# Performance work log

Hardware: AMD Instinct MI355X
Metric: run time of the kernel (lower is better)

The kernel has to match this reference:

```python
import jax, jax.numpy as jnp
import numpy as np

NB, H = 4, 16
EPS = 1e-5


def _ln(x, w=None, b=None):
    m = jnp.mean(x, -1, keepdims=True)
    v = jnp.var(x, -1, keepdims=True)
    y = (x - m) * jax.lax.rsqrt(v + EPS)
    if w is not None:
        y = y * w
    if b is not None:
        y = y + b
    return y


def _ada_ln(a, s, ln_s_w, w_gamma, w_beta):
    # AF3 Algorithm 26: a <- sigmoid(Lin(LN_nobias(s))) * LN_noaffine(a) + Lin(LN_nobias(s))
    a_n = _ln(a)
    s_n = _ln(s, ln_s_w)
    return jax.nn.sigmoid(s_n @ w_gamma) * a_n + s_n @ w_beta


def setup_inputs():
    key = jax.random.key(0)
    B, S, c_a, c_s, c_z = 1, 1024, 768, 384, 128
    n_hidden = 2 * c_a  # expansion factor n=2
    ks = iter(jax.random.split(key, 40))

    def rn(shape, scale=1.0):
        return scale * jax.random.normal(next(ks), shape, dtype=jnp.float32)

    p = 0.02
    return {
        "a": rn((B, S, c_a)),
        "s": rn((B, S, c_s)),
        "z": rn((B, S, S, c_z)),
        "beta": rn((B, S, S, H)),
        # per-block AttentionPairBias params (stacked over NB blocks)
        "ln_s_w_attn": jnp.ones((NB, c_s)),
        "wg_attn": rn((NB, c_s, c_a), p),
        "wb_attn": rn((NB, c_s, c_a), p),
        "wq": rn((NB, c_a, c_a), p),
        "bq": jnp.zeros((NB, c_a)),
        "wk": rn((NB, c_a, c_a), p),
        "wv": rn((NB, c_a, c_a), p),
        "ln_z_w": jnp.ones((NB, c_z)),
        "ln_z_b": jnp.zeros((NB, c_z)),
        "wpb": rn((NB, c_z, H), p),
        "wgate": rn((NB, c_a, c_a), p),
        "wo": rn((NB, c_a, c_a), p),
        "wsg_attn": rn((NB, c_s, c_a), p),
        "bsg_attn": -2.0 * jnp.ones((NB, c_a)),
        # per-block ConditionedTransitionBlock params
        "ln_s_w_tr": jnp.ones((NB, c_s)),
        "wg_tr": rn((NB, c_s, c_a), p),
        "wb_tr": rn((NB, c_s, c_a), p),
        "w_swish": rn((NB, c_a, n_hidden), p),
        "w_gate2": rn((NB, c_a, n_hidden), p),
        "wsg_tr": rn((NB, c_s, c_a), p),
        "bsg_tr": -2.0 * jnp.ones((NB, c_a)),
        "w_out": rn((NB, n_hidden, c_a), p),
    }


def reference(a, s, z, beta, ln_s_w_attn, wg_attn, wb_attn, wq, bq, wk, wv,
              ln_z_w, ln_z_b, wpb, wgate, wo, wsg_attn, bsg_attn,
              ln_s_w_tr, wg_tr, wb_tr, w_swish, w_gate2, wsg_tr, bsg_tr, w_out):
    B, S, c_a = a.shape
    d = c_a // H
    scale = 1.0 / jnp.sqrt(jnp.float32(d))
    for i in range(NB):
        # --- AttentionPairBias (AF3 Alg 24) ---
        ah = _ada_ln(a, s, ln_s_w_attn[i], wg_attn[i], wb_attn[i])
        q = (ah @ wq[i] + bq[i]).reshape(B, S, H, d)
        k = (ah @ wk[i]).reshape(B, S, H, d)
        v = (ah @ wv[i]).reshape(B, S, H, d)
        zb = _ln(z, ln_z_w[i], ln_z_b[i]) @ wpb[i]  # [B,S,S,H] pair bias
        scores = jnp.einsum('bihd,bjhd->bhij', q, k) * scale \
                 + jnp.transpose(zb + beta, (0, 3, 1, 2))
        attn = jax.nn.softmax(scores, axis=-1)
        o = jnp.einsum('bhij,bjhd->bihd', attn, v)
        g = jax.nn.sigmoid(ah @ wgate[i]).reshape(B, S, H, d)
        att_out = (g * o).reshape(B, S, c_a) @ wo[i]
        b_attn = jax.nn.sigmoid(s @ wsg_attn[i] + bsg_attn[i]) * att_out
        # --- ConditionedTransitionBlock (AF3 Alg 25, SwiGLU) ---
        th = _ada_ln(a, s, ln_s_w_tr[i], wg_tr[i], wb_tr[i])
        hidden = jax.nn.silu(th @ w_swish[i]) * (th @ w_gate2[i])
        tr = jax.nn.sigmoid(s @ wsg_tr[i] + bsg_tr[i]) * (hidden @ w_out[i])
        a = b_attn + tr
    return a
```

## Files before the change

### kernel.cpp

```cpp
#include <hip/hip_runtime.h>
#include <hip/hip_bf16.h>

typedef __hip_bfloat16 bf16;
typedef __attribute__((ext_vector_type(8))) short s8v;
typedef __attribute__((ext_vector_type(4))) float f4v;

constexpr int S = 1024, CA = 768, CS = 384, CZ = 128, NHID = 1536;
constexpr int NBLK = 4, NHEAD = 16, DH = 48;
constexpr float EPS = 1e-5f;

#define DEV static __device__ __forceinline__

DEV float sigmoidf_(float x) { return 1.0f / (1.0f + __expf(-x)); }

DEV f4v mfma16(s8v a, s8v b, f4v c) {
  return __builtin_amdgcn_mfma_f32_16x16x32_bf16(a, b, c, 0, 0, 0);
}

union U8 { s8v s; bf16 h[8]; };
union U4 { uint2 u; bf16 h[4]; };

DEV float wred_sum(float v) {
#pragma unroll
  for (int o = 32; o; o >>= 1) v += __shfl_xor(v, o);
  return v;
}

__global__ __launch_bounds__(256) void rowln_s(const float* __restrict__ x,
                                               bf16* __restrict__ s_hat,
                                               bf16* __restrict__ s_bf) {
  constexpr int C = CS, C4 = C / 4;
  __shared__ float red[8];
  const int t = threadIdx.x;
  const size_t row = blockIdx.x;
  float4 v = make_float4(0.f, 0.f, 0.f, 0.f);
  if (t < C4) v = ((const float4*)(x + row * C))[t];
  float sum = v.x + v.y + v.z + v.w;
  float sq = v.x * v.x + v.y * v.y + v.z * v.z + v.w * v.w;
  sum = wred_sum(sum); sq = wred_sum(sq);
  const int wv = t >> 6;
  if ((t & 63) == 0) { red[2 * wv] = sum; red[2 * wv + 1] = sq; }
  __syncthreads();
  sum = red[0] + red[2] + red[4] + red[6];
  sq = red[1] + red[3] + red[5] + red[7];
  const float m = sum / C;
  const float rstd = rsqrtf(sq / C - m * m + EPS);
  if (t < C4) {
    U4 oh, ob_;
    oh.h[0] = __float2bfloat16((v.x - m) * rstd); oh.h[1] = __float2bfloat16((v.y - m) * rstd);
    oh.h[2] = __float2bfloat16((v.z - m) * rstd); oh.h[3] = __float2bfloat16((v.w - m) * rstd);
    ob_.h[0] = __float2bfloat16(v.x); ob_.h[1] = __float2bfloat16(v.y);
    ob_.h[2] = __float2bfloat16(v.z); ob_.h[3] = __float2bfloat16(v.w);
    *(uint2*)(s_hat + row * C + 4 * t) = oh.u;
    *(uint2*)(s_bf + row * C + 4 * t) = ob_.u;
  }
}

__global__ __launch_bounds__(256) void ln_adaln2(const float* __restrict__ a,
                                                 const bf16* __restrict__ ada,
                                                 bf16* __restrict__ ah_attn,
                                                 bf16* __restrict__ ah_tr) {
  __shared__ float red[8];
  const int t = threadIdx.x;
  const size_t row = blockIdx.x;
  float4 v = make_float4(0.f, 0.f, 0.f, 0.f);
  if (t < 192) v = ((const float4*)(a + row * CA))[t];
  float sum = v.x + v.y + v.z + v.w;
  float sq = v.x * v.x + v.y * v.y + v.z * v.z + v.w * v.w;
  sum = wred_sum(sum); sq = wred_sum(sq);
  const int wv = t >> 6;
  if ((t & 63) == 0) { red[2 * wv] = sum; red[2 * wv + 1] = sq; }
  __syncthreads();
  sum = red[0] + red[2] + red[4] + red[6];
  sq = red[1] + red[3] + red[5] + red[7];
  const float m = sum / CA;
  const float rstd = rsqrtf(sq / CA - m * m + EPS);
  if (t < 192) {
    const float an[4] = {(v.x - m) * rstd, (v.y - m) * rstd, (v.z - m) * rstd, (v.w - m) * rstd};
    const bf16* ar = ada + row * 12288 + 4 * t;
    U4 g1, b1, g2, b2, o1, o2;
    g1.u = *(const uint2*)(ar);
    b1.u = *(const uint2*)(ar + 768);
    g2.u = *(const uint2*)(ar + 1536);
    b2.u = *(const uint2*)(ar + 2304);
#pragma unroll
    for (int j = 0; j < 4; ++j) {
      o1.h[j] = __float2bfloat16(sigmoidf_(__bfloat162float(g1.h[j])) * an[j] + __bfloat162float(b1.h[j]));
      o2.h[j] = __float2bfloat16(sigmoidf_(__bfloat162float(g2.h[j])) * an[j] + __bfloat162float(b2.h[j]));
    }
    *(uint2*)(ah_attn + row * CA + 4 * t) = o1.u;
    *(uint2*)(ah_tr + row * CA + 4 * t) = o2.u;
  }
}

struct TGroup {
  const float* src[6];
  bf16* dst[6];
  const float* cs[6];
  long dstZ[6];
};

__global__ __launch_bounds__(256) void transpose_grp(TGroup g, int K, int N, int csZ) {
  __shared__ float tile[32][33];
  const int z = blockIdx.z, wsel = z >> 2, blk = z & 3;
  const float* src = g.src[wsel] + (size_t)blk * K * N;
  bf16* dst = g.dst[wsel] + (size_t)blk * g.dstZ[wsel];
  const float* cs = g.cs[wsel];
  const int k0 = blockIdx.y * 32, n0 = blockIdx.x * 32;
  const int tx = threadIdx.x & 31, ty = threadIdx.x >> 5;
#pragma unroll
  for (int q = 0; q < 4; ++q) {
    const int k = k0 + ty + 8 * q;
    float v = src[(size_t)k * N + n0 + tx];
    if (cs) v *= cs[(size_t)blk * csZ + k];
    tile[ty + 8 * q][tx] = v;
  }
  __syncthreads();
#pragma unroll
  for (int q = 0; q < 4; ++q)
    dst[(size_t)(n0 + ty + 8 * q) * K + k0 + tx] = __float2bfloat16(tile[tx][ty + 8 * q]);
}

__global__ __launch_bounds__(256) void prep_w2(const float* __restrict__ ln_z_w,
                                               const float* __restrict__ ln_z_b,
                                               const float* __restrict__ wpb,
                                               bf16* __restrict__ W2T,
                                               float* __restrict__ bias2) {
  const int t = threadIdx.x;
  for (int f = t; f < 64 * CZ; f += 256) {
    const int col = f >> 7, c = f & 127, blk = col >> 4, h = col & 15;
    W2T[f] = __float2bfloat16(ln_z_w[blk * CZ + c] * wpb[(blk * CZ + c) * NHEAD + h]);
  }
  if (t < 64) {
    const int blk = t >> 4, h = t & 15;
    float sum = 0.f;
    for (int c = 0; c < CZ; ++c)
      sum += ln_z_b[blk * CZ + c] * wpb[(blk * CZ + c) * NHEAD + h];
    bias2[t] = sum;
  }
}

__global__ __launch_bounds__(256) void prep_biases(const float* __restrict__ bq,
                                                   const float* __restrict__ bsg_attn,
                                                   const float* __restrict__ bsg_tr,
                                                   float* __restrict__ biasQKVG,
                                                   float* __restrict__ biasSG) {
  const int t = blockIdx.x * 256 + threadIdx.x;
  if (t < 4 * 3072) {
    const int b = t / 3072, c = t % 3072;
    biasQKVG[t] = (c < 768) ? bq[b * 768 + c] : 0.f;
  }
  if (t < 6144) {
    const int b = t / 1536, c = t % 1536;
    biasSG[t] = (c < 768) ? bsg_attn[b * 768 + c] : bsg_tr[b * 768 + c - 768];
  }
}

__global__ __launch_bounds__(256) void zbias_kernel(const float* __restrict__ z,
                                                    const float* __restrict__ beta,
                                                    const bf16* __restrict__ W2T,
                                                    const float* __restrict__ bias2,
                                                    bf16* __restrict__ bias_all) {
  __shared__ s8v zt8[64 * 16];
  __shared__ s8v w2s[64 * 16];
  __shared__ float betas[64][17];
  __shared__ float bias2s[64];
  __shared__ bf16 obuf[64][72];
  const int t = threadIdx.x;
  const int i = blockIdx.y, j0 = blockIdx.x * 64;
#pragma unroll
  for (int q = 0; q < 4; ++q) {
    const int u = q * 256 + t;
    const int row = u >> 4, sl = u & 15;
    w2s[row * 16 + (sl ^ (row & 7))] = *(const s8v*)(W2T + row * CZ + sl * 8);
  }
  if (t < 64) bias2s[t] = bias2[t];
  {
    const int j = t >> 2, h4 = t & 3;
    const float4 bv = *(const float4*)(beta + ((size_t)i * S + j0 + j) * NHEAD + 4 * h4);
    betas[j][4 * h4 + 0] = bv.x; betas[j][4 * h4 + 1] = bv.y;
    betas[j][4 * h4 + 2] = bv.z; betas[j][4 * h4 + 3] = bv.w;
  }
  {
    const int p = t >> 2, q = t & 3;
    const float* zr = z + ((size_t)i * S + j0 + p) * CZ + q * 32;
    float vals[32];
    float sum = 0.f, sq = 0.f;
#pragma unroll
    for (int k4 = 0; k4 < 8; ++k4) {
      const float4 xv = *(const float4*)(zr + 4 * k4);
      vals[4 * k4 + 0] = xv.x; vals[4 * k4 + 1] = xv.y;
      vals[4 * k4 + 2] = xv.z; vals[4 * k4 + 3] = xv.w;
      sum += xv.x + xv.y + xv.z + xv.w;
      sq += xv.x * xv.x + xv.y * xv.y + xv.z * xv.z + xv.w * xv.w;
    }
    sum += __shfl_xor(sum, 1); sum += __shfl_xor(sum, 2);
    sq += __shfl_xor(sq, 1); sq += __shfl_xor(sq, 2);
    const float m = sum / CZ;
    const float rstd = rsqrtf(sq / CZ - m * m + EPS);
#pragma unroll
    for (int u = 0; u < 4; ++u) {
      U8 pk;
#pragma unroll
      for (int e = 0; e < 8; ++e) pk.h[e] = __float2bfloat16((vals[8 * u + e] - m) * rstd);
      const int cu = 4 * q + u;
      zt8[p * 16 + (cu ^ (p & 7))] = pk.s;
    }
  }
  __syncthreads();
  const int lane = t & 63, wid = t >> 6;
  const int wr = wid >> 1, wc = wid & 1;
  const int ln = lane & 15, lq = lane >> 4;
  f4v acc[2][2] = {};
#pragma unroll
  for (int kk = 0; kk < 4; ++kk) {
    const int sl = (lq + 4 * kk) ^ (ln & 7);
    s8v a[2], b[2];
#pragma unroll
    for (int mi = 0; mi < 2; ++mi) a[mi] = zt8[(32 * wr + 16 * mi + ln) * 16 + sl];
#pragma unroll
    for (int ni = 0; ni < 2; ++ni) b[ni] = w2s[(32 * wc + 16 * ni + ln) * 16 + sl];
#pragma unroll
    for (int mi = 0; mi < 2; ++mi)
#pragma unroll
      for (int ni = 0; ni < 2; ++ni) acc[mi][ni] = mfma16(a[mi], b[ni], acc[mi][ni]);
  }
#pragma unroll
  for (int mi = 0; mi < 2; ++mi)
#pragma unroll
    for (int ni = 0; ni < 2; ++ni) {
      const int col = 32 * wc + 16 * ni + ln;
      const int jb = 32 * wr + 16 * mi + 4 * lq;
      U4 o4;
#pragma unroll
      for (int r = 0; r < 4; ++r)
        o4.h[r] = __float2bfloat16(acc[mi][ni][r] + bias2s[col] + betas[jb + r][col & 15]);
      *(uint2*)&obuf[col][jb] = o4.u;
    }
  __syncthreads();
  {
    const int oc = t >> 2, js = (t & 3) * 16;
    bf16* dp = bias_all + (size_t)oc * S * S + (size_t)i * S + j0 + js;
    *(s8v*)dp = *(const s8v*)&obuf[oc][js];
    *(s8v*)(dp + 8) = *(const s8v*)&obuf[oc][js + 8];
  }
}

DEV void stC(float* p, float v) { *p = v; }
DEV void stC(bf16* p, float v) { *p = __float2bfloat16(v); }

template <int ACT, typename OT>
__global__ __launch_bounds__(256) void gemm_nt(const bf16* __restrict__ A0, int lda0,
                                               const bf16* __restrict__ Bt,
                                               const float* __restrict__ bias,
                                               OT* __restrict__ C, int M, int N, int K) {
  __shared__ s8v As[128 * 8];
  __shared__ s8v Bs[128 * 8];
  const int t = threadIdx.x;
  const int lane = t & 63, wid = t >> 6;
  const int wr = wid >> 1, wc = wid & 1;
  const int ln = lane & 15, lq = lane >> 4;
  const int m0 = blockIdx.y * 128, n0 = blockIdx.x * 128;
  int rowS[4], slS[4], swz[4];
#pragma unroll
  for (int q = 0; q < 4; ++q) {
    const int u = q * 256 + t;
    rowS[q] = u >> 3; slS[q] = u & 7;
    swz[q] = rowS[q] * 8 + (slS[q] ^ (rowS[q] & 7));
  }
  f4v acc[4][4] = {};
  s8v ra[4], rb[4];
#pragma unroll
  for (int q = 0; q < 4; ++q) {
    ra[q] = *(const s8v*)(A0 + (size_t)(m0 + rowS[q]) * lda0 + slS[q] * 8);
    rb[q] = *(const s8v*)(Bt + (size_t)(n0 + rowS[q]) * K + slS[q] * 8);
  }
  for (int ks = 0;;) {
    __syncthreads();
#pragma unroll
    for (int q = 0; q < 4; ++q) { As[swz[q]] = ra[q]; Bs[swz[q]] = rb[q]; }
    const int ksn = ks + 64;
    if (ksn < K) {
#pragma unroll
      for (int q = 0; q < 4; ++q) {
        ra[q] = *(const s8v*)(A0 + (size_t)(m0 + rowS[q]) * lda0 + ksn + slS[q] * 8);
        rb[q] = *(const s8v*)(Bt + (size_t)(n0 + rowS[q]) * K + ksn + slS[q] * 8);
      }
    }
    __syncthreads();
#pragma unroll
    for (int kk = 0; kk < 2; ++kk) {
      const int sl = (lq + 4 * kk) ^ (ln & 7);
      s8v a[4], b[4];
#pragma unroll
      for (int mi = 0; mi < 4; ++mi) a[mi] = As[(64 * wr + 16 * mi + ln) * 8 + sl];
#pragma unroll
      for (int ni = 0; ni < 4; ++ni) b[ni] = Bs[(64 * wc + 16 * ni + ln) * 8 + sl];
#pragma unroll
      for (int mi = 0; mi < 4; ++mi)
#pragma unroll
        for (int ni = 0; ni < 4; ++ni) acc[mi][ni] = mfma16(a[mi], b[ni], acc[mi][ni]);
    }
    ks = ksn;
    if (ks >= K) break;
  }
#pragma unroll
  for (int ni = 0; ni < 4; ++ni) {
    const int n = n0 + 64 * wc + 16 * ni + ln;
    const float bv = bias ? bias[n] : 0.f;
#pragma unroll
    for (int mi = 0; mi < 4; ++mi) {
      const int mb = m0 + 64 * wr + 16 * mi + 4 * lq;
#pragma unroll
      for (int r = 0; r < 4; ++r) {
        float v = acc[mi][ni][r] + bv;
        if (ACT == 1) v = sigmoidf_(v);
        stC(&C[(size_t)(mb + r) * N + n], v);
      }
    }
  }
}

struct GemmPairArgs {
  const bf16* A0[2]; int lda0[2];
  const bf16* A1[2]; int lda1[2];
  const bf16* Bt[2];
  const float* bias[2];
  bf16* C[2];
  int K[2]; int amode[2];
  bf16* vT;
};

DEV s8v combineRT(s8v x, s8v y, int amode) {
  U8 ux, uy, r;
  ux.s = x; uy.s = y;
#pragma unroll
  for (int j = 0; j < 8; ++j) {
    const float fx = __bfloat162float(ux.h[j]);
    const float fy = __bfloat162float(uy.h[j]);
    const float tt = sigmoidf_(fx);
    r.h[j] = __float2bfloat16((amode == 2 ? fx * tt : tt) * fy);
  }
  return r.s;
}

__global__ __launch_bounds__(256) void gemm_pair(GemmPairArgs ga, int N) {
  __shared__ s8v As[128 * 8];
  __shared__ s8v Bs[128 * 8];
  const int z = blockIdx.z;
  const bf16* A0 = ga.A0[z]; const int lda0 = ga.lda0[z];
  const bf16* A1 = ga.A1[z]; const int lda1 = ga.lda1[z];
  const bf16* Bt = ga.Bt[z];
  const float* bias = ga.bias[z];
  bf16* C = ga.C[z];
  const int K = ga.K[z], amode = ga.amode[z];
  const int t = threadIdx.x;
  const int lane = t & 63, wid = t >> 6;
  const int wr = wid >> 1, wc = wid & 1;
  const int ln = lane & 15, lq = lane >> 4;
  const int m0 = blockIdx.y * 128, n0 = blockIdx.x * 128;
  int rowS[4], slS[4], swz[4];
#pragma unroll
  for (int q = 0; q < 4; ++q) {
    const int u = q * 256 + t;
    rowS[q] = u >> 3; slS[q] = u & 7;
    swz[q] = rowS[q] * 8 + (slS[q] ^ (rowS[q] & 7));
  }
  f4v acc[4][4] = {};
  s8v ra[4], ra2[4], rb[4];
#pragma unroll
  for (int q = 0; q < 4; ++q) {
    ra[q] = *(const s8v*)(A0 + (size_t)(m0 + rowS[q]) * lda0 + slS[q] * 8);
    if (amode != 0) ra2[q] = *(const s8v*)(A1 + (size_t)(m0 + rowS[q]) * lda1 + slS[q] * 8);
    rb[q] = *(const s8v*)(Bt + (size_t)(n0 + rowS[q]) * K + slS[q] * 8);
  }
  for (int ks = 0;;) {
    __syncthreads();
#pragma unroll
    for (int q = 0; q < 4; ++q) {
      As[swz[q]] = (amode == 0) ? ra[q] : combineRT(ra[q], ra2[q], amode);
      Bs[swz[q]] = rb[q];
    }
    const int ksn = ks + 64;
    if (ksn < K) {
#pragma unroll
      for (int q = 0; q < 4; ++q) {
        ra[q] = *(const s8v*)(A0 + (size_t)(m0 + rowS[q]) * lda0 + ksn + slS[q] * 8);
        if (amode != 0) ra2[q] = *(const s8v*)(A1 + (size_t)(m0 + rowS[q]) * lda1 + ksn + slS[q] * 8);
        rb[q] = *(const s8v*)(Bt + (size_t)(n0 + rowS[q]) * K + ksn + slS[q] * 8);
      }
    }
    __syncthreads();
#pragma unroll
    for (int kk = 0; kk < 2; ++kk) {
      const int sl = (lq + 4 * kk) ^ (ln & 7);
      s8v a[4], b[4];
#pragma unroll
      for (int mi = 0; mi < 4; ++mi) a[mi] = As[(64 * wr + 16 * mi + ln) * 8 + sl];
#pragma unroll
      for (int ni = 0; ni < 4; ++ni) b[ni] = Bs[(64 * wc + 16 * ni + ln) * 8 + sl];
#pragma unroll
      for (int mi = 0; mi < 4; ++mi)
#pragma unroll
        for (int ni = 0; ni < 4; ++ni) acc[mi][ni] = mfma16(a[mi], b[ni], acc[mi][ni]);
    }
    ks = ksn;
    if (ks >= K) break;
  }
  const bool vdiv = (ga.vT != nullptr) && (z == 0) && (n0 >= 1536) && (n0 < 2304);
#pragma unroll
  for (int ni = 0; ni < 4; ++ni) {
    const int n = n0 + 64 * wc + 16 * ni + ln;
    const float bv = bias ? bias[n] : 0.f;
#pragma unroll
    for (int mi = 0; mi < 4; ++mi) {
      const int mb = m0 + 64 * wr + 16 * mi + 4 * lq;
      if (vdiv) {
        U4 o4;
#pragma unroll
        for (int r = 0; r < 4; ++r) o4.h[r] = __float2bfloat16(acc[mi][ni][r] + bv);
        *(uint2*)(ga.vT + (size_t)(n - 1536) * S + mb) = o4.u;
      } else {
#pragma unroll
        for (int r = 0; r < 4; ++r)
          C[(size_t)(mb + r) * N + n] = __float2bfloat16(acc[mi][ni][r] + bv);
      }
    }
  }
}

__global__ __launch_bounds__(256) void flash_attn(const bf16* __restrict__ qkvg,
                                                  const bf16* __restrict__ vT,
                                                  const bf16* __restrict__ bias_all,
                                                  bf16* __restrict__ ob, int blk) {
  __shared__ s8v Qs[64 * 8];
  __shared__ s8v Ks[2][64 * 8];
  __shared__ s8v Vs[2][48 * 8];
  __shared__ s8v Bs[2][64 * 8];
  __shared__ bf16 PwB[4 * 1024];
  __shared__ float facL[4][16];
  __shared__ float linvL[4][16];
  const int t = threadIdx.x;
  const int lane = t & 63, w = t >> 6;
  const int ln = lane & 15, lq = lane >> 4;
  const int h = blockIdx.y, i0 = blockIdx.x * 64;
  const bf16* bp = bias_all + (size_t)(blk * NHEAD + h) * S * S;
  const float scale = 0.14433756729740643f;

#pragma unroll
  for (int uu = 0; uu < 2; ++uu) {
    const int u = t + 256 * uu, row = u >> 3, sl = u & 7;
    s8v qv{};
    if (sl < 6) qv = *(const s8v*)(qkvg + (size_t)(i0 + row) * 3072 + h * DH + sl * 8);
    Qs[row * 8 + (sl ^ (row & 7))] = qv;
  }

  s8v kr[2], br[2], vr0{}, vr1{};
  auto prefetch = [&](int jt) {
    const int j0 = jt * 64;
#pragma unroll
    for (int uu = 0; uu < 2; ++uu) {
      const int u = t + 256 * uu, row = u >> 3, sl = u & 7;
      s8v kv{};
      if (sl < 6) kv = *(const s8v*)(qkvg + (size_t)(j0 + row) * 3072 + 768 + h * DH + sl * 8);
      kr[uu] = kv;
      br[uu] = *(const s8v*)(bp + (size_t)(i0 + row) * S + j0 + sl * 8);
    }
    { const int d = t >> 3, sl = t & 7;
      vr0 = *(const s8v*)(vT + (size_t)(h * DH + d) * S + j0 + sl * 8); }
    if (t < 128) {
      const int u = 256 + t, d = u >> 3, sl = u & 7;
      vr1 = *(const s8v*)(vT + (size_t)(h * DH + d) * S + j0 + sl * 8);
    }
  };
  auto store_tiles = [&](int pb) {
#pragma unroll
    for (int uu = 0; uu < 2; ++uu) {
      const int u = t + 256 * uu, row = u >> 3, sl = u & 7;
      const int ph = row * 8 + (sl ^ (row & 7));
      Ks[pb][ph] = kr[uu];
      Bs[pb][ph] = br[uu];
    }
    { const int d = t >> 3, sl = t & 7;
      Vs[pb][d * 8 + (sl ^ (d & 7))] = vr0; }
    if (t < 128) {
      const int u = 256 + t, d = u >> 3, sl = u & 7;
      Vs[pb][d * 8 + (sl ^ (d & 7))] = vr1;
    }
  };

  float m_run = -3e30f, l_run = 0.f;
  f4v acc_o[3] = {};
  bf16* pw = PwB + w * 1024;

  prefetch(0);
  for (int jt = 0; jt < 16; ++jt) {
    const int pb = jt & 1;
    __syncthreads();
    store_tiles(pb);
    __syncthreads();
    if (jt < 15) prefetch(jt + 1);
    float p[4][4];
    float tmax = -3e30f;
#pragma unroll
    for (int ja = 0; ja < 4; ++ja) {
      f4v accs = {};
#pragma unroll
      for (int ks2 = 0; ks2 < 2; ++ks2) {
        const int sl = (lq + 4 * ks2) ^ (ln & 7);
        const s8v a = Ks[pb][(16 * ja + ln) * 8 + sl];
        const s8v b = Qs[(16 * w + ln) * 8 + sl];
        accs = mfma16(a, b, accs);
      }
      const int jq = 4 * ja + lq;
      const int pu = jq >> 1;
      U4 bv;
      bv.u = *(const uint2*)((const bf16*)(&Bs[pb][0]) +
                             (((16 * w + ln) * 8 + (pu ^ (ln & 7))) * 8 + (jq & 1) * 4));
#pragma unroll
      for (int r = 0; r < 4; ++r) {
        p[ja][r] = accs[r] * scale + __bfloat162float(bv.h[r]);
        tmax = fmaxf(tmax, p[ja][r]);
      }
    }
    tmax = fmaxf(tmax, __shfl_xor(tmax, 16));
    tmax = fmaxf(tmax, __shfl_xor(tmax, 32));
    const float m_new = fmaxf(m_run, tmax);
    const float fac = __expf(m_run - m_new);
    m_run = m_new;
    float psum = 0.f;
#pragma unroll
    for (int ja = 0; ja < 4; ++ja)
#pragma unroll
      for (int r = 0; r < 4; ++r) {
        p[ja][r] = __expf(p[ja][r] - m_new);
        psum += p[ja][r];
      }
    psum += __shfl_xor(psum, 16);
    psum += __shfl_xor(psum, 32);
    l_run = l_run * fac + psum;
    if (lq == 0) facL[w][ln] = fac;
#pragma unroll
    for (int ja = 0; ja < 4; ++ja) {
      const int ju = 4 * ja + lq;
      const int ph = ju ^ ((ln & 7) << 1);
      U4 pk;
#pragma unroll
      for (int r = 0; r < 4; ++r) pk.h[r] = __float2bfloat16(p[ja][r]);
      *(uint2*)(pw + ln * 64 + ph * 4) = pk.u;
    }
    asm volatile("s_waitcnt lgkmcnt(0)" ::: "memory");
    __builtin_amdgcn_sched_barrier(0);
    const float4 fv = *(const float4*)&facL[w][4 * lq];
#pragma unroll
    for (int ni = 0; ni < 3; ++ni) {
      acc_o[ni][0] *= fv.x; acc_o[ni][1] *= fv.y;
      acc_o[ni][2] *= fv.z; acc_o[ni][3] *= fv.w;
    }
#pragma unroll
    for (int ks2 = 0; ks2 < 2; ++ks2) {
      const int pu0 = (2 * lq + 8 * ks2) ^ ((ln & 7) << 1);
      const s8v pa = *(const s8v*)(pw + ln * 64 + pu0 * 4);
      const int slv = (lq + 4 * ks2) ^ (ln & 7);
#pragma unroll
      for (int ni = 0; ni < 3; ++ni) {
        const s8v vb = Vs[pb][(16 * ni + ln) * 8 + slv];
        acc_o[ni] = mfma16(pa, vb, acc_o[ni]);
      }
    }
  }
  if (lq == 0) linvL[w][ln] = 1.0f / l_run;
  asm volatile("s_waitcnt lgkmcnt(0)" ::: "memory");
  __builtin_amdgcn_sched_barrier(0);
  const float4 lv = *(const float4*)&linvL[w][4 * lq];
  const float lvr[4] = {lv.x, lv.y, lv.z, lv.w};
#pragma unroll
  for (int ni = 0; ni < 3; ++ni)
#pragma unroll
    for (int r = 0; r < 4; ++r) {
      const int m = i0 + 16 * w + 4 * lq + r;
      ob[(size_t)m * CA + h * DH + 16 * ni + ln] = __float2bfloat16(acc_o[ni][r] * lvr[r]);
    }
}

__global__ __launch_bounds__(256) void ew_final(const float* __restrict__ sg,
                                                const bf16* __restrict__ att,
                                                const bf16* __restrict__ tr,
                                                float* __restrict__ out) {
  const int i = blockIdx.x * 256 + threadIdx.x;
  const int row = i / 192, col = (i % 192) * 4;
  const float4 sa = *(const float4*)(sg + (size_t)row * 6144 + col);
  const float4 st = *(const float4*)(sg + (size_t)row * 6144 + 768 + col);
  U4 av, tv;
  av.u = *(const uint2*)(att + (size_t)row * CA + col);
  tv.u = *(const uint2*)(tr + (size_t)row * CA + col);
  float4 o;
  o.x = sa.x * __bfloat162float(av.h[0]) + st.x * __bfloat162float(tv.h[0]);
  o.y = sa.y * __bfloat162float(av.h[1]) + st.y * __bfloat162float(tv.h[1]);
  o.z = sa.z * __bfloat162float(av.h[2]) + st.z * __bfloat162float(tv.h[2]);
  o.w = sa.w * __bfloat162float(av.h[3]) + st.w * __bfloat162float(tv.h[3]);
  *(float4*)(out + (size_t)row * CA + col) = o;
}

__global__ void fill_kernel(float* p, int n, float v) {
  const int i = blockIdx.x * 256 + threadIdx.x;
  if (i < n) p[i] = v;
}

extern "C" void kernel_launch(void* const* d_in, const int* in_sizes, int n_in,
                              void* d_out, int out_size, void* d_ws, size_t ws_size,
                              hipStream_t stream) {
  (void)in_sizes; (void)n_in;
  const float* a_in = (const float*)d_in[0];
  const float* s_in = (const float*)d_in[1];
  const float* z_in = (const float*)d_in[2];
  const float* beta = (const float*)d_in[3];
  const float* ln_s_w_attn = (const float*)d_in[4];
  const float* wg_attn = (const float*)d_in[5];
  const float* wb_attn = (const float*)d_in[6];
  const float* wq = (const float*)d_in[7];
  const float* bq = (const float*)d_in[8];
  const float* wk = (const float*)d_in[9];
  const float* wv = (const float*)d_in[10];
  const float* ln_z_w = (const float*)d_in[11];
  const float* ln_z_b = (const float*)d_in[12];
  const float* wpb = (const float*)d_in[13];
  const float* wgate = (const float*)d_in[14];
  const float* wo = (const float*)d_in[15];
  const float* wsg_attn = (const float*)d_in[16];
  const float* bsg_attn = (const float*)d_in[17];
  const float* ln_s_w_tr = (const float*)d_in[18];
  const float* wg_tr = (const float*)d_in[19];
  const float* wb_tr = (const float*)d_in[20];
  const float* w_swish = (const float*)d_in[21];
  const float* w_gate2 = (const float*)d_in[22];
  const float* wsg_tr = (const float*)d_in[23];
  const float* bsg_tr = (const float*)d_in[24];
  const float* w_out = (const float*)d_in[25];

  char* wp = (char*)d_ws;
  size_t used = 0;
  auto alloc = [&](size_t bytes) -> void* {
    void* p = wp + used;
    used += (bytes + 255) & ~(size_t)255;
    return p;
  };
  bf16* bias_all = (bf16*)alloc((size_t)64 * S * S * 2);
  bf16* WT_ada = (bf16*)alloc((size_t)4 * 3072 * 384 * 2);
  bf16* WT_sg = (bf16*)alloc((size_t)4 * 1536 * 384 * 2);
  bf16* WT_qkvg = (bf16*)alloc((size_t)4 * 3072 * 768 * 2);
  bf16* WT_wo = (bf16*)alloc((size_t)4 * 768 * 768 * 2);
  bf16* WT_mlp = (bf16*)alloc((size_t)4 * 3072 * 768 * 2);
  bf16* WT_wout = (bf16*)alloc((size_t)4 * 768 * 1536 * 2);
  float* biasQKVG = (float*)alloc(4 * 3072 * 4);
  float* biasSG = (float*)alloc(6144 * 4);
  bf16* W2T = (bf16*)alloc(64 * 128 * 2);
  float* bias2 = (float*)alloc(64 * 4);
  bf16* ada_all = (bf16*)alloc((size_t)S * 12288 * 2);
  float* sg_all = (float*)alloc((size_t)S * 6144 * 4);
  bf16* s_hat = (bf16*)alloc((size_t)S * CS * 2);
  bf16* s_bf = (bf16*)alloc((size_t)S * CS * 2);
  float* a_buf = (float*)alloc((size_t)S * CA * 4);
  bf16* ah_attn = (bf16*)alloc((size_t)S * CA * 2);
  bf16* ah_tr = (bf16*)alloc((size_t)S * CA * 2);
  bf16* qkvg = (bf16*)alloc((size_t)S * 3072 * 2);
  bf16* vT = (bf16*)alloc((size_t)CA * S * 2);
  bf16* ob = (bf16*)alloc((size_t)S * CA * 2);
  bf16* att = (bf16*)alloc((size_t)S * CA * 2);
  bf16* swg = (bf16*)alloc((size_t)S * 3072 * 2);
  bf16* trout = (bf16*)alloc((size_t)S * CA * 2);
  if (used > ws_size) {
    fill_kernel<<<(out_size + 255) / 256, 256, 0, stream>>>((float*)d_out, out_size, 12345.0f);
    return;
  }

  const dim3 B256(256);

  prep_w2<<<1, B256, 0, stream>>>(ln_z_w, ln_z_b, wpb, W2T, bias2);
  prep_biases<<<48, B256, 0, stream>>>(bq, bsg_attn, bsg_tr, biasQKVG, biasSG);

  {
    TGroup g{};
    g.src[0] = wg_attn;  g.dst[0] = WT_ada + (size_t)0 * 384;    g.cs[0] = ln_s_w_attn; g.dstZ[0] = 3072 * 384;
    g.src[1] = wb_attn;  g.dst[1] = WT_ada + (size_t)768 * 384;  g.cs[1] = ln_s_w_attn; g.dstZ[1] = 3072 * 384;
    g.src[2] = wg_tr;    g.dst[2] = WT_ada + (size_t)1536 * 384; g.cs[2] = ln_s_w_tr;   g.dstZ[2] = 3072 * 384;
    g.src[3] = wb_tr;    g.dst[3] = WT_ada + (size_t)2304 * 384; g.cs[3] = ln_s_w_tr;   g.dstZ[3] = 3072 * 384;
    g.src[4] = wsg_attn; g.dst[4] = WT_sg + (size_t)0 * 384;     g.cs[4] = nullptr;     g.dstZ[4] = 1536 * 384;
    g.src[5] = wsg_tr;   g.dst[5] = WT_sg + (size_t)768 * 384;   g.cs[5] = nullptr;     g.dstZ[5] = 1536 * 384;
    transpose_grp<<<dim3(24, 12, 24), B256, 0, stream>>>(g, 384, 768, CS);
  }
  {
    TGroup g{};
    g.src[0] = wq;    g.dst[0] = WT_qkvg + (size_t)0 * 768;    g.dstZ[0] = 3072 * 768;
    g.src[1] = wk;    g.dst[1] = WT_qkvg + (size_t)768 * 768;  g.dstZ[1] = 3072 * 768;
    g.src[2] = wv;    g.dst[2] = WT_qkvg + (size_t)1536 * 768; g.dstZ[2] = 3072 * 768;
    g.src[3] = wgate; g.dst[3] = WT_qkvg + (size_t)2304 * 768; g.dstZ[3] = 3072 * 768;
    g.src[4] = wo;    g.dst[4] = WT_wo;                        g.dstZ[4] = 768 * 768;
    transpose_grp<<<dim3(24, 24, 20), B256, 0, stream>>>(g, 768, 768, 0);
  }
  {
    TGroup g{};
    g.src[0] = w_swish; g.dst[0] = WT_mlp + (size_t)0 * 768;    g.dstZ[0] = 3072 * 768;
    g.src[1] = w_gate2; g.dst[1] = WT_mlp + (size_t)1536 * 768; g.dstZ[1] = 3072 * 768;
    transpose_grp<<<dim3(48, 24, 8), B256, 0, stream>>>(g, 768, 1536, 0);
  }
  {
    TGroup g{};
    g.src[0] = w_out; g.dst[0] = WT_wout; g.dstZ[0] = 768 * 1536;
    transpose_grp<<<dim3(24, 48, 4), B256, 0, stream>>>(g, 1536, 768, 0);
  }

  rowln_s<<<S, B256, 0, stream>>>(s_in, s_hat, s_bf);
  zbias_kernel<<<dim3(16, 1024), B256, 0, stream>>>(z_in, beta, W2T, bias2, bias_all);

  gemm_nt<0, bf16><<<dim3(96, 8), B256, 0, stream>>>(s_hat, 384, WT_ada, nullptr, ada_all, S, 12288, 384);
  gemm_nt<1, float><<<dim3(48, 8), B256, 0, stream>>>(s_bf, 384, WT_sg, biasSG, sg_all, S, 6144, 384);

  const float* a_cur = a_in;
  for (int b = 0; b < NBLK; ++b) {
    ln_adaln2<<<S, B256, 0, stream>>>(a_cur, ada_all + (size_t)b * 3072, ah_attn, ah_tr);
    {
      GemmPairArgs ga{};
      ga.A0[0] = ah_attn; ga.lda0[0] = 768; ga.A1[0] = nullptr; ga.lda1[0] = 0;
      ga.Bt[0] = WT_qkvg + (size_t)b * 3072 * 768; ga.bias[0] = biasQKVG + b * 3072;
      ga.C[0] = qkvg; ga.K[0] = 768; ga.amode[0] = 0;
      ga.A0[1] = ah_tr; ga.lda0[1] = 768; ga.A1[1] = nullptr; ga.lda1[1] = 0;
      ga.Bt[1] = WT_mlp + (size_t)b * 3072 * 768; ga.bias[1] = nullptr;
      ga.C[1] = swg; ga.K[1] = 768; ga.amode[1] = 0;
      ga.vT = vT;
      gemm_pair<<<dim3(24, 8, 2), B256, 0, stream>>>(ga, 3072);
    }
    flash_attn<<<dim3(16, 16), B256, 0, stream>>>(qkvg, vT, bias_all, ob, b);
    {
      GemmPairArgs ga{};
      ga.A0[0] = qkvg + 2304; ga.lda0[0] = 3072; ga.A1[0] = ob; ga.lda1[0] = 768;
      ga.Bt[0] = WT_wo + (size_t)b * 768 * 768; ga.bias[0] = nullptr;
      ga.C[0] = att; ga.K[0] = 768; ga.amode[0] = 1;
      ga.A0[1] = swg; ga.lda0[1] = 3072; ga.A1[1] = swg + 1536; ga.lda1[1] = 3072;
      ga.Bt[1] = WT_wout + (size_t)b * 768 * 1536; ga.bias[1] = nullptr;
      ga.C[1] = trout; ga.K[1] = 1536; ga.amode[1] = 2;
      ga.vT = nullptr;
      gemm_pair<<<dim3(6, 8, 2), B256, 0, stream>>>(ga, 768);
    }
    float* a_next = (b == NBLK - 1) ? (float*)d_out : a_buf;
    ew_final<<<768, B256, 0, stream>>>(sg_all + (size_t)b * 1536, att, trout, a_next);
    a_cur = a_next;
  }
}
```

Before: 666.8 us.

## Use direct global-to-LDS double-buffered GEMM, merge precompute GEMMs, shrink attention tiles

```diff
diff --git a/kernel.cpp b/kernel.cpp
--- a/kernel.cpp
+++ b/kernel.cpp
@@ -15,6 +15,11 @@
 
 DEV f4v mfma16(s8v a, s8v b, f4v c) {
   return __builtin_amdgcn_mfma_f32_16x16x32_bf16(a, b, c, 0, 0, 0);
+}
+
+DEV void gld_lds16(const void* g, void* l) {
+  __builtin_amdgcn_global_load_lds((const __attribute__((address_space(1))) void*)g,
+                                   (__attribute__((address_space(3))) void*)l, 16, 0, 0);
 }
 
 union U8 { s8v s; bf16 h[8]; };
@@ -246,76 +251,95 @@
   }
 }
 
-DEV void stC(float* p, float v) { *p = v; }
-DEV void stC(bf16* p, float v) { *p = __float2bfloat16(v); }
-
-template <int ACT, typename OT>
-__global__ __launch_bounds__(256) void gemm_nt(const bf16* __restrict__ A0, int lda0,
-                                               const bf16* __restrict__ Bt,
-                                               const float* __restrict__ bias,
-                                               OT* __restrict__ C, int M, int N, int K) {
-  __shared__ s8v As[128 * 8];
-  __shared__ s8v Bs[128 * 8];
+struct Gemm2Args {
+  const bf16* A0[2]; int lda0[2];
+  const bf16* Bt[2];
+  const float* bias[2];
+  void* C[2];
+  int K[2];
+  int nb[2];
+  int outMode[2];
+  int N[2];
+  bf16* vT;
+};
+
+__global__ __launch_bounds__(256) void gemm2(Gemm2Args ga) {
+  const int z = blockIdx.z;
+  if ((int)blockIdx.x >= ga.nb[z]) return;
+  __shared__ s8v As[2][1024];
+  __shared__ s8v Bs[2][1024];
+  const bf16* A0 = ga.A0[z]; const int lda0 = ga.lda0[z];
+  const bf16* Bt = ga.Bt[z];
+  const int K = ga.K[z], N = ga.N[z];
   const int t = threadIdx.x;
   const int lane = t & 63, wid = t >> 6;
   const int wr = wid >> 1, wc = wid & 1;
   const int ln = lane & 15, lq = lane >> 4;
   const int m0 = blockIdx.y * 128, n0 = blockIdx.x * 128;
-  int rowS[4], slS[4], swz[4];
+  int rowA[4], colx[4];
 #pragma unroll
   for (int q = 0; q < 4; ++q) {
-    const int u = q * 256 + t;
-    rowS[q] = u >> 3; slS[q] = u & 7;
-    swz[q] = rowS[q] * 8 + (slS[q] ^ (rowS[q] & 7));
-  }
+    const int u = q * 256 + t, row = u >> 3, slp = u & 7;
+    rowA[q] = row; colx[q] = (slp ^ (row & 7)) * 8;
+  }
+  auto stage = [&](int ks, int buf) {
+#pragma unroll
+    for (int q = 0; q < 4; ++q) {
+      gld_lds16(A0 + (size_t)(m0 + rowA[q]) * lda0 + ks + colx[q], &As[buf][q * 256 + wid * 64]);
+      gld_lds16(Bt + (size_t)(n0 + rowA[q]) * K + ks + colx[q], &Bs[buf][q * 256 + wid * 64]);
+    }
+  };
   f4v acc[4][4] = {};
-  s8v ra[4], rb[4];
-#pragma unroll
-  for (int q = 0; q < 4; ++q) {
-    ra[q] = *(const s8v*)(A0 + (size_t)(m0 + rowS[q]) * lda0 + slS[q] * 8);
-    rb[q] = *(const s8v*)(Bt + (size_t)(n0 + rowS[q]) * K + slS[q] * 8);
-  }
+  stage(0, 0);
+  __syncthreads();
+  int cur = 0;
   for (int ks = 0;;) {
-    __syncthreads();
-#pragma unroll
-    for (int q = 0; q < 4; ++q) { As[swz[q]] = ra[q]; Bs[swz[q]] = rb[q]; }
     const int ksn = ks + 64;
-    if (ksn < K) {
-#pragma unroll
-      for (int q = 0; q < 4; ++q) {
-        ra[q] = *(const s8v*)(A0 + (size_t)(m0 + rowS[q]) * lda0 + ksn + slS[q] * 8);
-        rb[q] = *(const s8v*)(Bt + (size_t)(n0 + rowS[q]) * K + ksn + slS[q] * 8);
-      }
-    }
-    __syncthreads();
+    if (ksn < K) stage(ksn, cur ^ 1);
+    __builtin_amdgcn_s_setprio(1);
 #pragma unroll
     for (int kk = 0; kk < 2; ++kk) {
       const int sl = (lq + 4 * kk) ^ (ln & 7);
       s8v a[4], b[4];
 #pragma unroll
-      for (int mi = 0; mi < 4; ++mi) a[mi] = As[(64 * wr + 16 * mi + ln) * 8 + sl];
-#pragma unroll
-      for (int ni = 0; ni < 4; ++ni) b[ni] = Bs[(64 * wc + 16 * ni + ln) * 8 + sl];
+      for (int mi = 0; mi < 4; ++mi) a[mi] = As[cur][(64 * wr + 16 * mi + ln) * 8 + sl];
+#pragma unroll
+      for (int ni = 0; ni < 4; ++ni) b[ni] = Bs[cur][(64 * wc + 16 * ni + ln) * 8 + sl];
 #pragma unroll
       for (int mi = 0; mi < 4; ++mi)
 #pragma unroll
         for (int ni = 0; ni < 4; ++ni) acc[mi][ni] = mfma16(a[mi], b[ni], acc[mi][ni]);
     }
+    __builtin_amdgcn_s_setprio(0);
     ks = ksn;
     if (ks >= K) break;
-  }
+    __syncthreads();
+    cur ^= 1;
+  }
+  const bool vdiv = (ga.vT != nullptr) && (z == 0) && (n0 >= 1536) && (n0 < 2304);
+  const int om = ga.outMode[z];
 #pragma unroll
   for (int ni = 0; ni < 4; ++ni) {
     const int n = n0 + 64 * wc + 16 * ni + ln;
-    const float bv = bias ? bias[n] : 0.f;
+    const float bv = ga.bias[z] ? ga.bias[z][n] : 0.f;
 #pragma unroll
     for (int mi = 0; mi < 4; ++mi) {
       const int mb = m0 + 64 * wr + 16 * mi + 4 * lq;
-#pragma unroll
-      for (int r = 0; r < 4; ++r) {
-        float v = acc[mi][ni][r] + bv;
-        if (ACT == 1) v = sigmoidf_(v);
-        stC(&C[(size_t)(mb + r) * N + n], v);
+      if (vdiv) {
+        U4 o4;
+#pragma unroll
+        for (int r = 0; r < 4; ++r) o4.h[r] = __float2bfloat16(acc[mi][ni][r] + bv);
+        *(uint2*)(ga.vT + (size_t)(n - 1536) * S + mb) = o4.u;
+      } else if (om == 0) {
+        bf16* C = (bf16*)ga.C[z];
+#pragma unroll
+        for (int r = 0; r < 4; ++r)
+          C[(size_t)(mb + r) * N + n] = __float2bfloat16(acc[mi][ni][r] + bv);
+      } else {
+        float* C = (float*)ga.C[z];
+#pragma unroll
+        for (int r = 0; r < 4; ++r)
+          C[(size_t)(mb + r) * N + n] = sigmoidf_(acc[mi][ni][r] + bv);
       }
     }
   }
@@ -328,7 +352,6 @@
   const float* bias[2];
   bf16* C[2];
   int K[2]; int amode[2];
-  bf16* vT;
 };
 
 DEV s8v combineRT(s8v x, s8v y, int amode) {
@@ -407,7 +430,6 @@
     ks = ksn;
     if (ks >= K) break;
   }
-  const bool vdiv = (ga.vT != nullptr) && (z == 0) && (n0 >= 1536) && (n0 < 2304);
 #pragma unroll
   for (int ni = 0; ni < 4; ++ni) {
     const int n = n0 + 64 * wc + 16 * ni + ln;
@@ -415,77 +437,75 @@
 #pragma unroll
     for (int mi = 0; mi < 4; ++mi) {
       const int mb = m0 + 64 * wr + 16 * mi + 4 * lq;
-      if (vdiv) {
-        U4 o4;
-#pragma unroll
-        for (int r = 0; r < 4; ++r) o4.h[r] = __float2bfloat16(acc[mi][ni][r] + bv);
-        *(uint2*)(ga.vT + (size_t)(n - 1536) * S + mb) = o4.u;
-      } else {
-#pragma unroll
-        for (int r = 0; r < 4; ++r)
-          C[(size_t)(mb + r) * N + n] = __float2bfloat16(acc[mi][ni][r] + bv);
-      }
-    }
-  }
-}
-
-__global__ __launch_bounds__(256) void flash_attn(const bf16* __restrict__ qkvg,
+#pragma unroll
+      for (int r = 0; r < 4; ++r)
+        C[(size_t)(mb + r) * N + n] = __float2bfloat16(acc[mi][ni][r] + bv);
+    }
+  }
+}
+
+__global__ __launch_bounds__(128) void flash_attn(const bf16* __restrict__ qkvg,
                                                   const bf16* __restrict__ vT,
                                                   const bf16* __restrict__ bias_all,
                                                   bf16* __restrict__ ob, int blk) {
-  __shared__ s8v Qs[64 * 8];
+  __shared__ s8v Qs[32 * 8];
   __shared__ s8v Ks[2][64 * 8];
   __shared__ s8v Vs[2][48 * 8];
-  __shared__ s8v Bs[2][64 * 8];
-  __shared__ bf16 PwB[4 * 1024];
-  __shared__ float facL[4][16];
-  __shared__ float linvL[4][16];
+  __shared__ s8v Bs[2][32 * 8];
+  __shared__ bf16 PwB[2 * 1024];
+  __shared__ float facL[2][16];
+  __shared__ float linvL[2][16];
   const int t = threadIdx.x;
   const int lane = t & 63, w = t >> 6;
   const int ln = lane & 15, lq = lane >> 4;
-  const int h = blockIdx.y, i0 = blockIdx.x * 64;
+  const int h = blockIdx.y, i0 = blockIdx.x * 32;
   const bf16* bp = bias_all + (size_t)(blk * NHEAD + h) * S * S;
   const float scale = 0.14433756729740643f;
 
 #pragma unroll
   for (int uu = 0; uu < 2; ++uu) {
-    const int u = t + 256 * uu, row = u >> 3, sl = u & 7;
+    const int u = t + 128 * uu, row = u >> 3, sl = u & 7;
     s8v qv{};
     if (sl < 6) qv = *(const s8v*)(qkvg + (size_t)(i0 + row) * 3072 + h * DH + sl * 8);
     Qs[row * 8 + (sl ^ (row & 7))] = qv;
   }
 
-  s8v kr[2], br[2], vr0{}, vr1{};
+  s8v kr[4], br[2], vr[3];
   auto prefetch = [&](int jt) {
     const int j0 = jt * 64;
 #pragma unroll
-    for (int uu = 0; uu < 2; ++uu) {
-      const int u = t + 256 * uu, row = u >> 3, sl = u & 7;
+    for (int uu = 0; uu < 4; ++uu) {
+      const int u = t + 128 * uu, row = u >> 3, sl = u & 7;
       s8v kv{};
       if (sl < 6) kv = *(const s8v*)(qkvg + (size_t)(j0 + row) * 3072 + 768 + h * DH + sl * 8);
       kr[uu] = kv;
+    }
+#pragma unroll
+    for (int uu = 0; uu < 2; ++uu) {
+      const int u = t + 128 * uu, row = u >> 3, sl = u & 7;
       br[uu] = *(const s8v*)(bp + (size_t)(i0 + row) * S + j0 + sl * 8);
     }
-    { const int d = t >> 3, sl = t & 7;
-      vr0 = *(const s8v*)(vT + (size_t)(h * DH + d) * S + j0 + sl * 8); }
-    if (t < 128) {
-      const int u = 256 + t, d = u >> 3, sl = u & 7;
-      vr1 = *(const s8v*)(vT + (size_t)(h * DH + d) * S + j0 + sl * 8);
+#pragma unroll
+    for (int uu = 0; uu < 3; ++uu) {
+      const int u = t + 128 * uu, d = u >> 3, sl = u & 7;
+      vr[uu] = *(const s8v*)(vT + (size_t)(h * DH + d) * S + j0 + sl * 8);
     }
   };
   auto store_tiles = [&](int pb) {
 #pragma unroll
+    for (int uu = 0; uu < 4; ++uu) {
+      const int u = t + 128 * uu, row = u >> 3, sl = u & 7;
+      Ks[pb][row * 8 + (sl ^ (row & 7))] = kr[uu];
+    }
+#pragma unroll
     for (int uu = 0; uu < 2; ++uu) {
-      const int u = t + 256 * uu, row = u >> 3, sl = u & 7;
-      const int ph = row * 8 + (sl ^ (row & 7));
-      Ks[pb][ph] = kr[uu];
-      Bs[pb][ph] = br[uu];
-    }
-    { const int d = t >> 3, sl = t & 7;
-      Vs[pb][d * 8 + (sl ^ (d & 7))] = vr0; }
-    if (t < 128) {
-      const int u = 256 + t, d = u >> 3, sl = u & 7;
-      Vs[pb][d * 8 + (sl ^ (d & 7))] = vr1;
+      const int u = t + 128 * uu, row = u >> 3, sl = u & 7;
+      Bs[pb][row * 8 + (sl ^ (row & 7))] = br[uu];
+    }
+#pragma unroll
+    for (int uu = 0; uu < 3; ++uu) {
+      const int u = t + 128 * uu, d = u >> 3, sl = u & 7;
+      Vs[pb][d * 8 + (sl ^ (d & 7))] = vr[uu];
     }
   };
 
@@ -502,6 +522,7 @@
     if (jt < 15) prefetch(jt + 1);
     float p[4][4];
     float tmax = -3e30f;
+    __builtin_amdgcn_s_setprio(1);
 #pragma unroll
     for (int ja = 0; ja < 4; ++ja) {
       f4v accs = {};
@@ -523,6 +544,7 @@
         tmax = fmaxf(tmax, p[ja][r]);
       }
     }
+    __builtin_amdgcn_s_setprio(0);
     tmax = fmaxf(tmax, __shfl_xor(tmax, 16));
     tmax = fmaxf(tmax, __shfl_xor(tmax, 32));
     const float m_new = fmaxf(m_run, tmax);
@@ -557,6 +579,7 @@
       acc_o[ni][0] *= fv.x; acc_o[ni][1] *= fv.y;
       acc_o[ni][2] *= fv.z; acc_o[ni][3] *= fv.w;
     }
+    __builtin_amdgcn_s_setprio(1);
 #pragma unroll
     for (int ks2 = 0; ks2 < 2; ++ks2) {
       const int pu0 = (2 * lq + 8 * ks2) ^ ((ln & 7) << 1);
@@ -568,6 +591,7 @@
         acc_o[ni] = mfma16(pa, vb, acc_o[ni]);
       }
     }
+    __builtin_amdgcn_s_setprio(0);
   }
   if (lq == 0) linvL[w][ln] = 1.0f / l_run;
   asm volatile("s_waitcnt lgkmcnt(0)" ::: "memory");
@@ -713,24 +737,31 @@
   rowln_s<<<S, B256, 0, stream>>>(s_in, s_hat, s_bf);
   zbias_kernel<<<dim3(16, 1024), B256, 0, stream>>>(z_in, beta, W2T, bias2, bias_all);
 
-  gemm_nt<0, bf16><<<dim3(96, 8), B256, 0, stream>>>(s_hat, 384, WT_ada, nullptr, ada_all, S, 12288, 384);
-  gemm_nt<1, float><<<dim3(48, 8), B256, 0, stream>>>(s_bf, 384, WT_sg, biasSG, sg_all, S, 6144, 384);
+  {
+    Gemm2Args ga{};
+    ga.A0[0] = s_hat; ga.lda0[0] = 384; ga.Bt[0] = WT_ada; ga.bias[0] = nullptr;
+    ga.C[0] = ada_all; ga.K[0] = 384; ga.nb[0] = 96; ga.outMode[0] = 0; ga.N[0] = 12288;
+    ga.A0[1] = s_bf; ga.lda0[1] = 384; ga.Bt[1] = WT_sg; ga.bias[1] = biasSG;
+    ga.C[1] = sg_all; ga.K[1] = 384; ga.nb[1] = 48; ga.outMode[1] = 1; ga.N[1] = 6144;
+    ga.vT = nullptr;
+    gemm2<<<dim3(96, 8, 2), B256, 0, stream>>>(ga);
+  }
 
   const float* a_cur = a_in;
   for (int b = 0; b < NBLK; ++b) {
     ln_adaln2<<<S, B256, 0, stream>>>(a_cur, ada_all + (size_t)b * 3072, ah_attn, ah_tr);
     {
-      GemmPairArgs ga{};
-      ga.A0[0] = ah_attn; ga.lda0[0] = 768; ga.A1[0] = nullptr; ga.lda1[0] = 0;
-      ga.Bt[0] = WT_qkvg + (size_t)b * 3072 * 768; ga.bias[0] = biasQKVG + b * 3072;
-      ga.C[0] = qkvg; ga.K[0] = 768; ga.amode[0] = 0;
-      ga.A0[1] = ah_tr; ga.lda0[1] = 768; ga.A1[1] = nullptr; ga.lda1[1] = 0;
-      ga.Bt[1] = WT_mlp + (size_t)b * 3072 * 768; ga.bias[1] = nullptr;
-      ga.C[1] = swg; ga.K[1] = 768; ga.amode[1] = 0;
+      Gemm2Args ga{};
+      ga.A0[0] = ah_attn; ga.lda0[0] = 768; ga.Bt[0] = WT_qkvg + (size_t)b * 3072 * 768;
+      ga.bias[0] = biasQKVG + b * 3072; ga.C[0] = qkvg; ga.K[0] = 768; ga.nb[0] = 24;
+      ga.outMode[0] = 0; ga.N[0] = 3072;
+      ga.A0[1] = ah_tr; ga.lda0[1] = 768; ga.Bt[1] = WT_mlp + (size_t)b * 3072 * 768;
+      ga.bias[1] = nullptr; ga.C[1] = swg; ga.K[1] = 768; ga.nb[1] = 24;
+      ga.outMode[1] = 0; ga.N[1] = 3072;
       ga.vT = vT;
-      gemm_pair<<<dim3(24, 8, 2), B256, 0, stream>>>(ga, 3072);
-    }
-    flash_attn<<<dim3(16, 16), B256, 0, stream>>>(qkvg, vT, bias_all, ob, b);
+      gemm2<<<dim3(24, 8, 2), B256, 0, stream>>>(ga);
+    }
+    flash_attn<<<dim3(32, 16), dim3(128), 0, stream>>>(qkvg, vT, bias_all, ob, b);
     {
       GemmPairArgs ga{};
       ga.A0[0] = qkvg + 2304; ga.lda0[0] = 3072; ga.A1[0] = ob; ga.lda1[0] = 768;
@@ -739,7 +770,6 @@
       ga.A0[1] = swg; ga.lda0[1] = 3072; ga.A1[1] = swg + 1536; ga.lda1[1] = 3072;
       ga.Bt[1] = WT_wout + (size_t)b * 768 * 1536; ga.bias[1] = nullptr;
       ga.C[1] = trout; ga.K[1] = 1536; ga.amode[1] = 2;
-      ga.vT = nullptr;
       gemm_pair<<<dim3(6, 8, 2), B256, 0, stream>>>(ga, 768);
     }
     float* a_next = (b == NBLK - 1) ? (float*)d_out : a_buf;
```

Measured after the change: 705.1 us. 5.7% more time.
